# Kernel optimization log

Hardware: AMD Instinct MI355X
Metric: run time of the kernel (lower is better)

The kernel has to match this reference:

```python
import jax, jax.numpy as jnp
import numpy as np

N, E, M, F, L = 50000, 800000, 50000, 64, 20
HID = 32
NEG_SLOPE = 0.2


def gatv2(x, src, dst, Wl, Wr, att, b, heads, outc):
    # PyG GATv2Conv (eval mode, dropout off), self-loops already in src/dst.
    n = x.shape[0]
    xl = (x @ Wl).reshape(n, heads, outc)
    xr = (x @ Wr).reshape(n, heads, outc)
    e = jax.nn.leaky_relu(xl[src] + xr[dst], NEG_SLOPE)          # [E, H, C]
    score = jnp.einsum('ehc,hc->eh', e, att)                      # [E, H]
    smax = jax.ops.segment_max(score, dst, num_segments=n)
    ex = jnp.exp(score - smax[dst])
    denom = jax.ops.segment_sum(ex, dst, num_segments=n)
    alpha = ex / denom[dst]                                       # scatter-softmax
    out = jax.ops.segment_sum(alpha[:, :, None] * xl[src], dst, num_segments=n)
    return out.reshape(n, heads * outc) + b


def setup_inputs() -> dict:
    key = jax.random.key(0)
    ks = jax.random.split(key, 32)
    d = {}
    d['x'] = jax.random.normal(ks[0], (N, 60), jnp.float32)
    d['lane_x'] = jax.random.normal(ks[1], (M, 2), jnp.float32)
    d['centerline'] = jax.random.normal(ks[2], (F, L, 2), jnp.float32)
    d['edge_index'] = jax.random.randint(ks[3], (2, E), 0, N)
    d['focal_idx'] = jax.random.randint(ks[4], (F,), 0, N)
    s = 0.1
    d['emb_W'] = jax.random.normal(ks[5], (60, HID)) * s
    d['emb_b'] = jnp.zeros((HID,))
    d['c1_Wl'] = jax.random.normal(ks[6], (HID, 4 * HID)) * s
    d['c1_Wr'] = jax.random.normal(ks[7], (HID, 4 * HID)) * s
    d['c1_att'] = jax.random.normal(ks[8], (4, HID)) * s
    d['c1_b'] = jnp.zeros((4 * HID,))
    d['c2_Wl'] = jax.random.normal(ks[9], (4 * HID, 4 * HID)) * s
    d['c2_Wr'] = jax.random.normal(ks[10], (4 * HID, 4 * HID)) * s
    d['c2_att'] = jax.random.normal(ks[11], (4, HID)) * s
    d['c2_b'] = jnp.zeros((4 * HID,))
    d['map_W'] = jax.random.normal(ks[12], (2, HID)) * s
    d['map_b'] = jnp.zeros((HID,))
    d['gg_Wl'] = jax.random.normal(ks[13], (4 * HID, HID)) * s
    d['gg_Wr'] = jax.random.normal(ks[14], (4 * HID, HID)) * s
    d['gg_att'] = jax.random.normal(ks[15], (1, HID)) * s
    d['gg_b'] = jnp.zeros((HID,))
    d['cl_W'] = jax.random.normal(ks[16], (2, HID)) * s
    d['cl_b'] = jnp.zeros((HID,))
    d['fc1_W'] = jax.random.normal(ks[17], (3 * HID, HID)) * s
    d['fc1_b'] = jnp.zeros((HID,))
    d['fc2_W'] = jax.random.normal(ks[18], (HID, HID // 2)) * s
    d['fc2_b'] = jnp.zeros((HID // 2,))
    d['fco_W'] = jax.random.normal(ks[19], (HID // 2, 60)) * s
    d['fco_b'] = jnp.zeros((60,))
    return d


def reference(x, lane_x, centerline, edge_index, focal_idx,
              emb_W, emb_b, c1_Wl, c1_Wr, c1_att, c1_b,
              c2_Wl, c2_Wr, c2_att, c2_b, map_W, map_b,
              gg_Wl, gg_Wr, gg_att, gg_b, cl_W, cl_b,
              fc1_W, fc1_b, fc2_W, fc2_b, fco_W, fco_b):
    n = x.shape[0]
    loops = jnp.arange(n)
    src = jnp.concatenate([edge_index[0], loops])  # PyG adds self-loops
    dst = jnp.concatenate([edge_index[1], loops])
    # agent encoder + subgraph (two GATv2 layers, heads=4, concat)
    h = jax.nn.relu(x @ emb_W + emb_b)                                   # [N,32]
    h = jax.nn.relu(gatv2(h, src, dst, c1_Wl, c1_Wr, c1_att, c1_b, 4, HID))
    agent_feat = jax.nn.relu(gatv2(h, src, dst, c2_Wl, c2_Wr, c2_att, c2_b, 4, HID))  # [N,128]
    # map branch (executable path: no lane edges -> plain embedding + mean pool)
    map_x = jax.nn.relu(lane_x @ map_W + map_b)                          # [M,32]
    map_global = jnp.mean(map_x, axis=0, keepdims=True)                  # [1,32]
    # global graph (heads=1)
    gf = jax.nn.relu(gatv2(agent_feat, src, dst, gg_Wl, gg_Wr, gg_att, gg_b, 1, HID))  # [N,32]
    focal = gf[focal_idx]                                                # [F,32]
    map_g = jnp.broadcast_to(map_global, (focal.shape[0], HID))
    cl = jnp.mean(centerline, axis=1) @ cl_W + cl_b                      # [F,32]
    comb = jnp.concatenate([focal, map_g, cl], axis=1)                   # [F,96]
    h = jax.nn.relu(comb @ fc1_W + fc1_b)
    h = jax.nn.relu(h @ fc2_W + fc2_b)
    return h @ fco_W + fco_b                                             # [F,60]
```

## Files before the change

kernel.cpp:

```cpp
#include <hip/hip_runtime.h>
#include <hip/hip_bf16.h>
#include <hip/hip_fp16.h>

typedef _Float16 half_t;
typedef _Float16 h8 __attribute__((ext_vector_type(8)));
typedef _Float16 h4v __attribute__((ext_vector_type(4)));
typedef _Float16 h2v __attribute__((ext_vector_type(2)));
typedef float f4v __attribute__((ext_vector_type(4)));

union H8u { h8 v; h2v h2[4]; _Float16 e[8]; };
union H4u { h4v v; h2v h2[2]; _Float16 e[4]; };

static inline int cdiv(long a, long b) { return (int)((a + b - 1) / b); }

__device__ __forceinline__ void fma4(float4& a, float s, const float4& w) {
    a.x += s * w.x; a.y += s * w.y; a.z += s * w.z; a.w += s * w.w;
}

__device__ __forceinline__ h8 hmax8(h8 a, h8 b) {
#if __has_builtin(__builtin_elementwise_max)
    return __builtin_elementwise_max(a, b);
#else
    h8 r;
#pragma unroll
    for (int j = 0; j < 8; ++j) r[j] = (a[j] > b[j]) ? a[j] : b[j];
    return r;
#endif
}
__device__ __forceinline__ h4v hmax4(h4v a, h4v b) {
#if __has_builtin(__builtin_elementwise_max)
    return __builtin_elementwise_max(a, b);
#else
    h4v r;
#pragma unroll
    for (int j = 0; j < 4; ++j) r[j] = (a[j] > b[j]) ? a[j] : b[j];
    return r;
#endif
}

__device__ __forceinline__ float dot2acc(h2v a, h2v b, float c) {
#if __has_builtin(__builtin_amdgcn_fdot2)
    return __builtin_amdgcn_fdot2(a, b, c, false);
#else
    return c + (float)a.x * (float)b.x + (float)a.y * (float)b.y;
#endif
}


template <int K4, int C4, int R>
__global__ __launch_bounds__(256) void gemm_t_h(
        const float* __restrict__ X, const float* __restrict__ W,
        const float* __restrict__ bias, half_t* __restrict__ Y,
        int Nr, int relu) {
    int idx = blockIdx.x * blockDim.x + threadIdx.x;
    int total = (Nr / R) * C4;
    if (idx >= total) return;
    int c4 = idx % C4;
    int n0 = (idx / C4) * R;
    const float4* __restrict__ Wv = (const float4*)W;
    const float4* __restrict__ Xv = (const float4*)X;
    float4 acc[R];
    float4 binit = bias ? ((const float4*)bias)[c4] : make_float4(0.f, 0.f, 0.f, 0.f);
#pragma unroll
    for (int r = 0; r < R; ++r) acc[r] = binit;
#pragma unroll 4
    for (int k4 = 0; k4 < K4; ++k4) {
        float4 w0 = Wv[(size_t)(4 * k4 + 0) * C4 + c4];
        float4 w1 = Wv[(size_t)(4 * k4 + 1) * C4 + c4];
        float4 w2 = Wv[(size_t)(4 * k4 + 2) * C4 + c4];
        float4 w3 = Wv[(size_t)(4 * k4 + 3) * C4 + c4];
#pragma unroll
        for (int r = 0; r < R; ++r) {
            float4 xv = Xv[(size_t)(n0 + r) * K4 + k4];
            fma4(acc[r], xv.x, w0); fma4(acc[r], xv.y, w1);
            fma4(acc[r], xv.z, w2); fma4(acc[r], xv.w, w3);
        }
    }
#pragma unroll
    for (int r = 0; r < R; ++r) {
        float4 o = acc[r];
        if (relu) {
            o.x = fmaxf(o.x, 0.f); o.y = fmaxf(o.y, 0.f);
            o.z = fmaxf(o.z, 0.f); o.w = fmaxf(o.w, 0.f);
        }
        h4v oh; oh.x = (half_t)o.x; oh.y = (half_t)o.y; oh.z = (half_t)o.z; oh.w = (half_t)o.w;
        ((h4v*)Y)[(size_t)(n0 + r) * C4 + c4] = oh;
    }
}


__global__ void wtrans(const float* __restrict__ c1l, const float* __restrict__ c1r,
                       const float* __restrict__ c2l, const float* __restrict__ c2r,
                       const float* __restrict__ ggl, const float* __restrict__ ggr,
                       const float* __restrict__ at1, const float* __restrict__ at2,
                       const float* __restrict__ atg, half_t* __restrict__ dst) {
    int idx = blockIdx.x * blockDim.x + threadIdx.x;
    if (idx >= 49440) return;
    if (idx >= 49152) {
        int j = idx - 49152;
        float v = (j < 128) ? at1[j] : (j < 256) ? at2[j - 128] : atg[j - 256];
        dst[idx] = (half_t)v;
        return;
    }
    const float* src; int K, loc;
    if (idx < 8192) {
        K = 32;
        if (idx < 4096) { src = c1l; loc = idx; } else { src = c1r; loc = idx - 4096; }
        int k = loc % K, c = loc / K;
        dst[idx] = (half_t)src[k * 128 + c];
    } else if (idx < 40960) {
        K = 128;
        if (idx < 24576) { src = c2l; loc = idx - 8192; } else { src = c2r; loc = idx - 24576; }
        int k = loc % K, c = loc / K;
        dst[idx] = (half_t)src[k * 128 + c];
    } else {
        K = 128;
        if (idx < 45056) { src = ggl; loc = idx - 40960; } else { src = ggr; loc = idx - 45056; }
        int k = loc % K, c = loc / K;
        dst[idx] = (half_t)src[k * 32 + c];
    }
}


template <int K, int C1>
__global__ __launch_bounds__(256) void mfma_dual(
        const half_t* __restrict__ Xh,
        const half_t* __restrict__ W1t, const half_t* __restrict__ W2t,
        half_t* __restrict__ Y1, half_t* __restrict__ Y2, int Nr) {
    constexpr int KT = K / 32;
    constexpr int NBC = (2 * C1) / 64;
    int wave = threadIdx.x >> 6, lane = threadIdx.x & 63;
    int bCol = blockIdx.x % NBC;
    int bRow = blockIdx.x / NBC;
    int rowBase = bRow * 128 + wave * 32;
    int colBase = bCol * 64;
    int m = lane & 15, quad = lane >> 4;

    f4v acc[2][4] = {};

    const half_t* bptr[4];
#pragma unroll
    for (int nt = 0; nt < 4; ++nt) {
        int gc = colBase + nt * 16 + m;
        bptr[nt] = (gc < C1) ? (W1t + (size_t)gc * K) : (W2t + (size_t)(gc - C1) * K);
    }
    int r0 = rowBase + m, r1 = rowBase + 16 + m;
    int r0c = (r0 < Nr) ? r0 : (Nr - 1);
    int r1c = (r1 < Nr) ? r1 : (Nr - 1);
    const half_t* a0p = Xh + (size_t)r0c * K + quad * 8;
    const half_t* a1p = Xh + (size_t)r1c * K + quad * 8;

#pragma unroll
    for (int kk = 0; kk < KT; ++kk) {
        h8 a0 = *(const h8*)(a0p + kk * 32);
        h8 a1 = *(const h8*)(a1p + kk * 32);
#pragma unroll
        for (int nt = 0; nt < 4; ++nt) {
            h8 b = *(const h8*)(bptr[nt] + kk * 32 + quad * 8);
            acc[0][nt] = __builtin_amdgcn_mfma_f32_16x16x32_f16(a0, b, acc[0][nt], 0, 0, 0);
            acc[1][nt] = __builtin_amdgcn_mfma_f32_16x16x32_f16(a1, b, acc[1][nt], 0, 0, 0);
        }
    }

#pragma unroll
    for (int mt = 0; mt < 2; ++mt) {
#pragma unroll
        for (int nt = 0; nt < 4; ++nt) {
            int gc = colBase + nt * 16 + m;
            half_t* Y = (gc < C1) ? (Y1 + gc) : (Y2 + (gc - C1));
#pragma unroll
            for (int r = 0; r < 4; ++r) {
                int gr = rowBase + mt * 16 + quad * 4 + r;
                if (gr < Nr) Y[(size_t)gr * C1] = (half_t)acc[mt][nt][r];
            }
        }
    }
}


__global__ void count_dst(const int* __restrict__ ei, int* __restrict__ counts,
                          int E, int Etot) {
    int e = blockIdx.x * blockDim.x + threadIdx.x;
    if (e >= Etot) return;
    int d = (e < E) ? ei[E + e] : (e - E);
    atomicAdd(&counts[d], 1);
}

#define SCAN_CH 2048

__global__ void reduce_chunks(const int* __restrict__ counts, int* __restrict__ partial, int N) {
    __shared__ int sh[256];
    int t = threadIdx.x, base = blockIdx.x * SCAN_CH + t * 8;
    int s = 0;
    for (int j = 0; j < 8; ++j) if (base + j < N) s += counts[base + j];
    sh[t] = s; __syncthreads();
    for (int off = 128; off >= 1; off >>= 1) {
        if (t < off) sh[t] += sh[t + off];
        __syncthreads();
    }
    if (t == 0) partial[blockIdx.x] = sh[0];
}

__global__ void scan_partials(int* __restrict__ partial, int nch) {
    if (threadIdx.x == 0 && blockIdx.x == 0) {
        int run = 0;
        for (int i = 0; i < nch; ++i) { int v = partial[i]; partial[i] = run; run += v; }
    }
}

__global__ void scan_chunks(const int* __restrict__ counts, const int* __restrict__ partial,
                            int* __restrict__ offsets, int N) {
    __shared__ int sh[256];
    int t = threadIdx.x, b = blockIdx.x, base = b * SCAN_CH + t * 8;
    int v[8], s = 0;
    for (int j = 0; j < 8; ++j) { v[j] = (base + j < N) ? counts[base + j] : 0; s += v[j]; }
    sh[t] = s; __syncthreads();
    for (int off = 1; off < 256; off <<= 1) {
        int x = (t >= off) ? sh[t - off] : 0;
        __syncthreads();
        sh[t] += x;
        __syncthreads();
    }
    int run = partial[b] + (t == 0 ? 0 : sh[t - 1]);
    for (int j = 0; j < 8; ++j) {
        if (base + j < N) offsets[base + j] = run;
        run += v[j];
    }
}

__global__ void fill_adj(const int* __restrict__ ei, const int* __restrict__ offsets,
                         int* __restrict__ cursor, int* __restrict__ adj, int E, int Etot) {
    int e = blockIdx.x * blockDim.x + threadIdx.x;
    if (e >= Etot) return;
    int s, d;
    if (e < E) { s = ei[e]; d = ei[E + e]; } else { s = e - E; d = s; }
    int pos = offsets[d] + atomicAdd(&cursor[d], 1);
    adj[pos] = s;
}


__global__ __launch_bounds__(256) void gat8_h4(
        const half_t* __restrict__ xl, const half_t* __restrict__ xr,
        const half_t* __restrict__ atth, const int* __restrict__ offsets,
        const int* __restrict__ counts, const int* __restrict__ adj,
        const float* __restrict__ bias, half_t* __restrict__ out, int N) {
    int wave = threadIdx.x >> 6, lane = threadIdx.x & 63;
    int g = lane >> 3, t = lane & 7;
    int d = blockIdx.x * 32 + wave * 8 + g;
    int dc = (d < N) ? d : (N - 1);
    int off = offsets[dc];
    int deg = (d < N) ? counts[dc] : 0;
    int dmax = deg;
    dmax = max(dmax, __shfl_xor(dmax, 8));
    dmax = max(dmax, __shfl_xor(dmax, 16));
    dmax = max(dmax, __shfl_xor(dmax, 32));

    const half_t* xrp = xr + (size_t)dc * 128 + t * 16;
    h8 xr_lo = *(const h8*)(xrp);
    h8 xr_hi = *(const h8*)(xrp + 8);
    H8u at_lo, at_hi;
    at_lo.v = *(const h8*)(atth + t * 16);
    at_hi.v = *(const h8*)(atth + t * 16 + 8);

    float acc[16];
#pragma unroll
    for (int j = 0; j < 16; ++j) acc[j] = 0.f;
    float lsum = 0.f;
    h8 c02;
#pragma unroll
    for (int j = 0; j < 8; ++j) c02[j] = (half_t)0.2f;

    for (int i = 0; i < dmax; ++i) {
        bool valid = (i < deg);
        int s = adj[off + (valid ? i : 0)];
        const half_t* xp = xl + (size_t)s * 128 + t * 16;
        H8u a_lo, a_hi;
        a_lo.v = *(const h8*)(xp);
        a_hi.v = *(const h8*)(xp + 8);
        h8 v_lo = a_lo.v + xr_lo;
        h8 v_hi = a_hi.v + xr_hi;
        H8u lk_lo, lk_hi;
        lk_lo.v = hmax8(v_lo, v_lo * c02);
        lk_hi.v = hmax8(v_hi, v_hi * c02);
        float p = 0.f;
#pragma unroll
        for (int j = 0; j < 4; ++j) p = dot2acc(lk_lo.h2[j], at_lo.h2[j], p);
#pragma unroll
        for (int j = 0; j < 4; ++j) p = dot2acc(lk_hi.h2[j], at_hi.h2[j], p);
        p += __shfl_xor(p, 1);
        float w = valid ? __expf(p) : 0.f;
        lsum += w;
#pragma unroll
        for (int j = 0; j < 8; ++j) acc[j] += w * (float)a_lo.e[j];
#pragma unroll
        for (int j = 0; j < 8; ++j) acc[8 + j] += w * (float)a_hi.e[j];
    }

    if (d < N) {
        float inv = 1.f / lsum;
        H8u o_lo, o_hi;
#pragma unroll
        for (int j = 0; j < 8; ++j)
            o_lo.e[j] = (half_t)fmaxf(acc[j] * inv + bias[t * 16 + j], 0.f);
#pragma unroll
        for (int j = 0; j < 8; ++j)
            o_hi.e[j] = (half_t)fmaxf(acc[8 + j] * inv + bias[t * 16 + 8 + j], 0.f);
        half_t* op = out + (size_t)d * 128 + t * 16;
        *(h8*)(op) = o_lo.v;
        *(h8*)(op + 8) = o_hi.v;
    }
}

__global__ __launch_bounds__(256) void gat8_h1(
        const half_t* __restrict__ xl, const half_t* __restrict__ xr,
        const half_t* __restrict__ atth, const int* __restrict__ offsets,
        const int* __restrict__ counts, const int* __restrict__ adj,
        const float* __restrict__ bias, float* __restrict__ out, int N) {
    int wave = threadIdx.x >> 6, lane = threadIdx.x & 63;
    int g = lane >> 3, t = lane & 7;
    int d = blockIdx.x * 32 + wave * 8 + g;
    int dc = (d < N) ? d : (N - 1);
    int off = offsets[dc];
    int deg = (d < N) ? counts[dc] : 0;
    int dmax = deg;
    dmax = max(dmax, __shfl_xor(dmax, 8));
    dmax = max(dmax, __shfl_xor(dmax, 16));
    dmax = max(dmax, __shfl_xor(dmax, 32));

    h4v xr4 = *(const h4v*)(xr + (size_t)dc * 32 + t * 4);
    H4u at4; at4.v = *(const h4v*)(atth + t * 4);

    float acc[4] = {0.f, 0.f, 0.f, 0.f};
    float lsum = 0.f;
    h4v c02;
#pragma unroll
    for (int j = 0; j < 4; ++j) c02[j] = (half_t)0.2f;

    for (int i = 0; i < dmax; ++i) {
        bool valid = (i < deg);
        int s = adj[off + (valid ? i : 0)];
        H4u a; a.v = *(const h4v*)(xl + (size_t)s * 32 + t * 4);
        h4v v = a.v + xr4;
        H4u lk; lk.v = hmax4(v, v * c02);
        float p = dot2acc(lk.h2[0], at4.h2[0], 0.f);
        p = dot2acc(lk.h2[1], at4.h2[1], p);
        p += __shfl_xor(p, 1);
        p += __shfl_xor(p, 2);
        p += __shfl_xor(p, 4);
        float w = valid ? __expf(p) : 0.f;
        lsum += w;
#pragma unroll
        for (int j = 0; j < 4; ++j) acc[j] += w * (float)a.e[j];
    }

    if (d < N) {
        float inv = 1.f / lsum;
        float4 o;
        o.x = fmaxf(acc[0] * inv + bias[t * 4 + 0], 0.f);
        o.y = fmaxf(acc[1] * inv + bias[t * 4 + 1], 0.f);
        o.z = fmaxf(acc[2] * inv + bias[t * 4 + 2], 0.f);
        o.w = fmaxf(acc[3] * inv + bias[t * 4 + 3], 0.f);
        *(float4*)(out + (size_t)d * 32 + t * 4) = o;
    }
}


__global__ void map_sum_kernel(const float* __restrict__ lane_x, const float* __restrict__ map_W,
                               const float* __restrict__ map_b, float* __restrict__ sums, int M) {
    __shared__ float s[32];
    if (threadIdx.x < 32) s[threadIdx.x] = 0.f;
    __syncthreads();
    int t = blockIdx.x * blockDim.x + threadIdx.x;
    int nth = gridDim.x * blockDim.x;
    int c = t & 31;
    float w0 = map_W[c], w1 = map_W[32 + c], bb = map_b[c];
    float acc = 0.f;
    for (int m = t >> 5; m < M; m += nth >> 5) {
        float v = lane_x[(long)m * 2] * w0 + lane_x[(long)m * 2 + 1] * w1 + bb;
        acc += fmaxf(v, 0.f);
    }
    atomicAdd(&s[c], acc);
    __syncthreads();
    if (threadIdx.x < 32) atomicAdd(&sums[threadIdx.x], s[threadIdx.x]);
}


__global__ void head_kernel(const float* __restrict__ gf, const int* __restrict__ focal_idx,
                            const float* __restrict__ map_sums, int M,
                            const float* __restrict__ centerline, int L,
                            const float* __restrict__ cl_W, const float* __restrict__ cl_b,
                            const float* __restrict__ fc1_W, const float* __restrict__ fc1_b,
                            const float* __restrict__ fc2_W, const float* __restrict__ fc2_b,
                            const float* __restrict__ fco_W, const float* __restrict__ fco_b,
                            float* __restrict__ out) {
    int f = blockIdx.x;
    int lane = threadIdx.x;
    __shared__ float s_comb[96];
    __shared__ float s_h1[32];
    __shared__ float s_h2[16];
    __shared__ float s_cl[2];

    float c0 = 0.f, c1 = 0.f;
    if (lane < L) {
        c0 = centerline[((long)f * L + lane) * 2 + 0];
        c1 = centerline[((long)f * L + lane) * 2 + 1];
    }
    for (int off = 32; off >= 1; off >>= 1) {
        c0 += __shfl_down(c0, off);
        c1 += __shfl_down(c1, off);
    }
    if (lane == 0) { s_cl[0] = c0 / (float)L; s_cl[1] = c1 / (float)L; }
    __syncthreads();

    int fi = focal_idx[f];
    if (lane < 32) {
        s_comb[lane] = gf[(long)fi * 32 + lane];
        s_comb[32 + lane] = map_sums[lane] / (float)M;
        s_comb[64 + lane] = s_cl[0] * cl_W[lane] + s_cl[1] * cl_W[32 + lane] + cl_b[lane];
    }
    __syncthreads();

    if (lane < 32) {
        float acc = fc1_b[lane];
        for (int k = 0; k < 96; ++k) acc += s_comb[k] * fc1_W[k * 32 + lane];
        s_h1[lane] = fmaxf(acc, 0.f);
    }
    __syncthreads();

    if (lane < 16) {
        float acc = fc2_b[lane];
        for (int k = 0; k < 32; ++k) acc += s_h1[k] * fc2_W[k * 16 + lane];
        s_h2[lane] = fmaxf(acc, 0.f);
    }
    __syncthreads();

    if (lane < 60) {
        float acc = fco_b[lane];
        for (int k = 0; k < 16; ++k) acc += s_h2[k] * fco_W[k * 60 + lane];
        out[(long)f * 60 + lane] = acc;
    }
}


extern "C" void kernel_launch(void* const* d_in, const int* in_sizes, int n_in,
                              void* d_out, int out_size, void* d_ws, size_t ws_size,
                              hipStream_t stream) {
    const float* x          = (const float*)d_in[0];
    const float* lane_x     = (const float*)d_in[1];
    const float* centerline = (const float*)d_in[2];
    const int*   ei         = (const int*)d_in[3];
    const int*   focal_idx  = (const int*)d_in[4];
    const float* emb_W = (const float*)d_in[5];
    const float* emb_b = (const float*)d_in[6];
    const float* c1_Wl = (const float*)d_in[7];
    const float* c1_Wr = (const float*)d_in[8];
    const float* c1_att = (const float*)d_in[9];
    const float* c1_b  = (const float*)d_in[10];
    const float* c2_Wl = (const float*)d_in[11];
    const float* c2_Wr = (const float*)d_in[12];
    const float* c2_att = (const float*)d_in[13];
    const float* c2_b  = (const float*)d_in[14];
    const float* map_W = (const float*)d_in[15];
    const float* map_b = (const float*)d_in[16];
    const float* gg_Wl = (const float*)d_in[17];
    const float* gg_Wr = (const float*)d_in[18];
    const float* gg_att = (const float*)d_in[19];
    const float* gg_b  = (const float*)d_in[20];
    const float* cl_W  = (const float*)d_in[21];
    const float* cl_b  = (const float*)d_in[22];
    const float* fc1_W = (const float*)d_in[23];
    const float* fc1_b = (const float*)d_in[24];
    const float* fc2_W = (const float*)d_in[25];
    const float* fc2_b = (const float*)d_in[26];
    const float* fco_W = (const float*)d_in[27];
    const float* fco_b = (const float*)d_in[28];

    const int N = in_sizes[0] / 60;
    const int M = in_sizes[1] / 2;
    const int F = in_sizes[4];
    const int L = in_sizes[2] / (F * 2);
    const int E = in_sizes[3] / 2;
    const int Etot = E + N;

    half_t* Xl_h = (half_t*)d_ws;
    half_t* Xr_h = Xl_h + (size_t)N * 128;
    half_t* H0_h = Xr_h + (size_t)N * 128;
    half_t* H1_h = H0_h + (size_t)N * 32;
    half_t* AF_h = H1_h + (size_t)N * 128;
    float*  GF_f = (float*)(AF_h + (size_t)N * 128);
    half_t* Wt   = (half_t*)(GF_f + (size_t)N * 32);
    int* counts  = (int*)(Wt + 49440);
    int* offsets = counts + N;
    int* cursor  = offsets + N;
    int* adj     = cursor + N;
    float* MAPS  = (float*)(adj + Etot);
    int* partial = (int*)(MAPS + 32);

    half_t* c1Wlt = Wt + 0;
    half_t* c1Wrt = Wt + 4096;
    half_t* c2Wlt = Wt + 8192;
    half_t* c2Wrt = Wt + 24576;
    half_t* ggWlt = Wt + 40960;
    half_t* ggWrt = Wt + 45056;
    half_t* att1h = Wt + 49152;
    half_t* att2h = Wt + 49280;
    half_t* attgh = Wt + 49408;

    const int BS = 256;
    const int nch = cdiv(N, SCAN_CH);
    const int rowBlocks = cdiv(N, 128);

    hipMemsetAsync(counts, 0, (size_t)N * sizeof(int), stream);
    hipMemsetAsync(cursor, 0, (size_t)N * sizeof(int), stream);
    count_dst<<<cdiv(Etot, BS), BS, 0, stream>>>(ei, counts, E, Etot);
    reduce_chunks<<<nch, 256, 0, stream>>>(counts, partial, N);
    scan_partials<<<1, 64, 0, stream>>>(partial, nch);
    scan_chunks<<<nch, 256, 0, stream>>>(counts, partial, offsets, N);
    fill_adj<<<cdiv(Etot, BS), BS, 0, stream>>>(ei, offsets, cursor, adj, E, Etot);

    wtrans<<<cdiv(49440, BS), BS, 0, stream>>>(c1_Wl, c1_Wr, c2_Wl, c2_Wr, gg_Wl, gg_Wr,
                                               c1_att, c2_att, gg_att, Wt);

    gemm_t_h<15, 8, 4><<<cdiv((long)(N / 4) * 8, BS), BS, 0, stream>>>(x, emb_W, emb_b, H0_h, N, 1);

    mfma_dual<32, 128><<<rowBlocks * 4, 256, 0, stream>>>(H0_h, c1Wlt, c1Wrt, Xl_h, Xr_h, N);
    gat8_h4<<<cdiv(N, 32), 256, 0, stream>>>(Xl_h, Xr_h, att1h, offsets, counts, adj, c1_b, H1_h, N);

    mfma_dual<128, 128><<<rowBlocks * 4, 256, 0, stream>>>(H1_h, c2Wlt, c2Wrt, Xl_h, Xr_h, N);
    gat8_h4<<<cdiv(N, 32), 256, 0, stream>>>(Xl_h, Xr_h, att2h, offsets, counts, adj, c2_b, AF_h, N);

    mfma_dual<128, 32><<<rowBlocks * 1, 256, 0, stream>>>(AF_h, ggWlt, ggWrt, Xl_h, Xr_h, N);
    gat8_h1<<<cdiv(N, 32), 256, 0, stream>>>(Xl_h, Xr_h, attgh, offsets, counts, adj, gg_b, GF_f, N);

    hipMemsetAsync(MAPS, 0, 32 * sizeof(float), stream);
    map_sum_kernel<<<64, BS, 0, stream>>>(lane_x, map_W, map_b, MAPS, M);

    head_kernel<<<F, 64, 0, stream>>>(GF_f, focal_idx, MAPS, M, centerline, L,
                                      cl_W, cl_b, fc1_W, fc1_b, fc2_W, fc2_b,
                                      fco_W, fco_b, (float*)d_out);
}
```

Measured before the change: 397.8 us.

## Sort destination nodes by degree to balance GAT wave loops

Builds a counting-sort permutation of destination nodes by in-degree (capped at 63) and has the three GAT aggregation kernels process nodes in that order. Eight nodes share a wave and loop up to the wave's largest degree, so grouping nodes of similar degree is meant to cut wasted iterations. It also seeds the fill cursor with the scan offsets, which removes a memset and an offsets load, and uses nontemporal stores for the adjacency array. In exchange it adds three small kernels, one of them a single-thread scan. Neighbouring destinations in a wave are no longer contiguous, so output writes and xr reads scatter.

```diff
diff --git a/kernel.cpp b/kernel.cpp
--- a/kernel.cpp
+++ b/kernel.cpp
@@ -201,15 +201,17 @@
     if (t == 0) partial[blockIdx.x] = sh[0];
 }
 
-__global__ void scan_partials(int* __restrict__ partial, int nch) {
-    if (threadIdx.x == 0 && blockIdx.x == 0) {
+__global__ void scan_partials(int* __restrict__ partial, int nch, int* __restrict__ dhist) {
+    int t = threadIdx.x;
+    if (t < 64) dhist[t] = 0;
+    if (t == 0) {
         int run = 0;
         for (int i = 0; i < nch; ++i) { int v = partial[i]; partial[i] = run; run += v; }
     }
 }
 
 __global__ void scan_chunks(const int* __restrict__ counts, const int* __restrict__ partial,
-                            int* __restrict__ offsets, int N) {
+                            int* __restrict__ offsets, int* __restrict__ cursor, int N) {
     __shared__ int sh[256];
     int t = threadIdx.x, b = blockIdx.x, base = b * SCAN_CH + t * 8;
     int v[8], s = 0;
@@ -223,19 +225,44 @@
     }
     int run = partial[b] + (t == 0 ? 0 : sh[t - 1]);
     for (int j = 0; j < 8; ++j) {
-        if (base + j < N) offsets[base + j] = run;
+        if (base + j < N) { offsets[base + j] = run; cursor[base + j] = run; }
         run += v[j];
     }
 }
 
-__global__ void fill_adj(const int* __restrict__ ei, const int* __restrict__ offsets,
-                         int* __restrict__ cursor, int* __restrict__ adj, int E, int Etot) {
+__global__ void fill_adj(const int* __restrict__ ei, int* __restrict__ cursor,
+                         int* __restrict__ adj, int E, int Etot) {
     int e = blockIdx.x * blockDim.x + threadIdx.x;
     if (e >= Etot) return;
     int s, d;
     if (e < E) { s = ei[e]; d = ei[E + e]; } else { s = e - E; d = s; }
-    int pos = offsets[d] + atomicAdd(&cursor[d], 1);
-    adj[pos] = s;
+    int pos = atomicAdd(&cursor[d], 1);
+    __builtin_nontemporal_store(s, &adj[pos]);
+}
+
+
+__global__ void dhist_k(const int* __restrict__ counts, int* __restrict__ dhist, int N) {
+    int i = blockIdx.x * blockDim.x + threadIdx.x;
+    if (i >= N) return;
+    atomicAdd(&dhist[min(counts[i], 63)], 1);
+}
+
+__global__ void dscan(const int* __restrict__ dhist, int* __restrict__ dbase,
+                      int* __restrict__ dstorder, int N, int Npad) {
+    int t = threadIdx.x;
+    if (t == 0) {
+        int run = 0;
+        for (int b = 0; b < 64; ++b) { dbase[b] = run; run += dhist[b]; }
+    }
+    if (N + t < Npad) dstorder[N + t] = -1;
+}
+
+__global__ void dscatter(const int* __restrict__ counts, int* __restrict__ dbase,
+                         int* __restrict__ dstorder, int N) {
+    int i = blockIdx.x * blockDim.x + threadIdx.x;
+    if (i >= N) return;
+    int p = atomicAdd(&dbase[min(counts[i], 63)], 1);
+    dstorder[p] = i;
 }
 
 
@@ -243,13 +270,15 @@
         const half_t* __restrict__ xl, const half_t* __restrict__ xr,
         const half_t* __restrict__ atth, const int* __restrict__ offsets,
         const int* __restrict__ counts, const int* __restrict__ adj,
+        const int* __restrict__ dstorder,
         const float* __restrict__ bias, half_t* __restrict__ out, int N) {
     int wave = threadIdx.x >> 6, lane = threadIdx.x & 63;
     int g = lane >> 3, t = lane & 7;
-    int d = blockIdx.x * 32 + wave * 8 + g;
-    int dc = (d < N) ? d : (N - 1);
+    int idx = blockIdx.x * 32 + wave * 8 + g;
+    int od = dstorder[idx];
+    int dc = (od >= 0) ? od : 0;
     int off = offsets[dc];
-    int deg = (d < N) ? counts[dc] : 0;
+    int deg = (od >= 0) ? counts[dc] : 0;
     int dmax = deg;
     dmax = max(dmax, __shfl_xor(dmax, 8));
     dmax = max(dmax, __shfl_xor(dmax, 16));
@@ -296,7 +325,7 @@
         for (int j = 0; j < 8; ++j) acc[8 + j] += w * (float)a_hi.e[j];
     }
 
-    if (d < N) {
+    if (od >= 0) {
         float inv = 1.f / lsum;
         H8u o_lo, o_hi;
 #pragma unroll
@@ -305,7 +334,7 @@
 #pragma unroll
         for (int j = 0; j < 8; ++j)
             o_hi.e[j] = (half_t)fmaxf(acc[8 + j] * inv + bias[t * 16 + 8 + j], 0.f);
-        half_t* op = out + (size_t)d * 128 + t * 16;
+        half_t* op = out + (size_t)od * 128 + t * 16;
         *(h8*)(op) = o_lo.v;
         *(h8*)(op + 8) = o_hi.v;
     }
@@ -315,13 +344,15 @@
         const half_t* __restrict__ xl, const half_t* __restrict__ xr,
         const half_t* __restrict__ atth, const int* __restrict__ offsets,
         const int* __restrict__ counts, const int* __restrict__ adj,
+        const int* __restrict__ dstorder,
         const float* __restrict__ bias, float* __restrict__ out, int N) {
     int wave = threadIdx.x >> 6, lane = threadIdx.x & 63;
     int g = lane >> 3, t = lane & 7;
-    int d = blockIdx.x * 32 + wave * 8 + g;
-    int dc = (d < N) ? d : (N - 1);
+    int idx = blockIdx.x * 32 + wave * 8 + g;
+    int od = dstorder[idx];
+    int dc = (od >= 0) ? od : 0;
     int off = offsets[dc];
-    int deg = (d < N) ? counts[dc] : 0;
+    int deg = (od >= 0) ? counts[dc] : 0;
     int dmax = deg;
     dmax = max(dmax, __shfl_xor(dmax, 8));
     dmax = max(dmax, __shfl_xor(dmax, 16));
@@ -353,14 +384,14 @@
         for (int j = 0; j < 4; ++j) acc[j] += w * (float)a.e[j];
     }
 
-    if (d < N) {
+    if (od >= 0) {
         float inv = 1.f / lsum;
         float4 o;
         o.x = fmaxf(acc[0] * inv + bias[t * 4 + 0], 0.f);
         o.y = fmaxf(acc[1] * inv + bias[t * 4 + 1], 0.f);
         o.z = fmaxf(acc[2] * inv + bias[t * 4 + 2], 0.f);
         o.w = fmaxf(acc[3] * inv + bias[t * 4 + 3], 0.f);
-        *(float4*)(out + (size_t)d * 32 + t * 4) = o;
+        *(float4*)(out + (size_t)od * 32 + t * 4) = o;
     }
 }
 
@@ -481,6 +512,7 @@
     const int L = in_sizes[2] / (F * 2);
     const int E = in_sizes[3] / 2;
     const int Etot = E + N;
+    const int Npad = cdiv(N, 32) * 32;
 
     half_t* Xl_h = (half_t*)d_ws;
     half_t* Xr_h = Xl_h + (size_t)N * 128;
@@ -493,7 +525,10 @@
     int* offsets = counts + N;
     int* cursor  = offsets + N;
     int* adj     = cursor + N;
-    float* MAPS  = (float*)(adj + Etot);
+    int* dstorder= adj + Etot;
+    int* dhist   = dstorder + Npad;
+    int* dbase   = dhist + 64;
+    float* MAPS  = (float*)(dbase + 64);
     int* partial = (int*)(MAPS + 32);
 
     half_t* c1Wlt = Wt + 0;
@@ -511,12 +546,14 @@
     const int rowBlocks = cdiv(N, 128);
 
     hipMemsetAsync(counts, 0, (size_t)N * sizeof(int), stream);
-    hipMemsetAsync(cursor, 0, (size_t)N * sizeof(int), stream);
     count_dst<<<cdiv(Etot, BS), BS, 0, stream>>>(ei, counts, E, Etot);
     reduce_chunks<<<nch, 256, 0, stream>>>(counts, partial, N);
-    scan_partials<<<1, 64, 0, stream>>>(partial, nch);
-    scan_chunks<<<nch, 256, 0, stream>>>(counts, partial, offsets, N);
-    fill_adj<<<cdiv(Etot, BS), BS, 0, stream>>>(ei, offsets, cursor, adj, E, Etot);
+    scan_partials<<<1, 64, 0, stream>>>(partial, nch, dhist);
+    scan_chunks<<<nch, 256, 0, stream>>>(counts, partial, offsets, cursor, N);
+    fill_adj<<<cdiv(Etot, BS), BS, 0, stream>>>(ei, cursor, adj, E, Etot);
+    dhist_k<<<cdiv(N, BS), BS, 0, stream>>>(counts, dhist, N);
+    dscan<<<1, 64, 0, stream>>>(dhist, dbase, dstorder, N, Npad);
+    dscatter<<<cdiv(N, BS), BS, 0, stream>>>(counts, dbase, dstorder, N);
 
     wtrans<<<cdiv(49440, BS), BS, 0, stream>>>(c1_Wl, c1_Wr, c2_Wl, c2_Wr, gg_Wl, gg_Wr,
                                                c1_att, c2_att, gg_att, Wt);
@@ -524,13 +561,13 @@
     gemm_t_h<15, 8, 4><<<cdiv((long)(N / 4) * 8, BS), BS, 0, stream>>>(x, emb_W, emb_b, H0_h, N, 1);
 
     mfma_dual<32, 128><<<rowBlocks * 4, 256, 0, stream>>>(H0_h, c1Wlt, c1Wrt, Xl_h, Xr_h, N);
-    gat8_h4<<<cdiv(N, 32), 256, 0, stream>>>(Xl_h, Xr_h, att1h, offsets, counts, adj, c1_b, H1_h, N);
+    gat8_h4<<<Npad / 32, 256, 0, stream>>>(Xl_h, Xr_h, att1h, offsets, counts, adj, dstorder, c1_b, H1_h, N);
 
     mfma_dual<128, 128><<<rowBlocks * 4, 256, 0, stream>>>(H1_h, c2Wlt, c2Wrt, Xl_h, Xr_h, N);
-    gat8_h4<<<cdiv(N, 32), 256, 0, stream>>>(Xl_h, Xr_h, att2h, offsets, counts, adj, c2_b, AF_h, N);
+    gat8_h4<<<Npad / 32, 256, 0, stream>>>(Xl_h, Xr_h, att2h, offsets, counts, adj, dstorder, c2_b, AF_h, N);
 
     mfma_dual<128, 32><<<rowBlocks * 1, 256, 0, stream>>>(AF_h, ggWlt, ggWrt, Xl_h, Xr_h, N);
-    gat8_h1<<<cdiv(N, 32), 256, 0, stream>>>(Xl_h, Xr_h, attgh, offsets, counts, adj, gg_b, GF_f, N);
+    gat8_h1<<<Npad / 32, 256, 0, stream>>>(Xl_h, Xr_h, attgh, offsets, counts, adj, dstorder, gg_b, GF_f, N);
 
     hipMemsetAsync(MAPS, 0, 32 * sizeof(float), stream);
     map_sum_kernel<<<64, BS, 0, stream>>>(lane_x, map_W, map_b, MAPS, M);
```

New measurement: 672.4 us. 1.69x slower.
